# Kernel tuning notes

Measured on AMD Instinct MI355X. Metric: run time of the kernel, lower is better.

Reference implementation:

```python
import jax, jax.numpy as jnp
import numpy as np

N_NODES = 100000
N_EDGES = 4800000


def gcn_conv(x, edge_index, W, b):
    """PyG GCNConv: add self-loops, symmetric deg^-1/2 normalization, scatter-add."""
    n = x.shape[0]
    loops = jnp.arange(n, dtype=edge_index.dtype)
    src = jnp.concatenate([edge_index[0], loops])  # [E+N] message sources
    dst = jnp.concatenate([edge_index[1], loops])  # [E+N] message targets
    deg = jax.ops.segment_sum(jnp.ones_like(dst, dtype=x.dtype), dst, num_segments=n)
    dinv = jnp.where(deg > 0, jax.lax.rsqrt(deg), 0.0)  # deg^{-1/2}, guard isolated nodes
    norm = dinv[src] * dinv[dst]                  # [E+N]
    h = x @ W                                      # [N, out] tiny GEMM
    msg = h[src] * norm[:, None]                   # gather + scale (memory bound)
    out = jax.ops.segment_sum(msg, dst, num_segments=n)  # scatter-add
    return out + b


def setup_inputs() -> dict:
    key = jax.random.key(0)
    k1, k2, k3, k4 = jax.random.split(key, 4)
    node_features = jax.random.normal(k1, (N_NODES, 1), dtype=jnp.float32)
    edge_index = jax.random.randint(k2, (2, N_EDGES), 0, N_NODES, dtype=jnp.int32)
    W1 = jax.random.normal(k3, (1, 16), dtype=jnp.float32) / jnp.sqrt(1.0)
    b1 = jnp.zeros((16,), dtype=jnp.float32)
    W2 = jax.random.normal(k4, (16, 2), dtype=jnp.float32) / jnp.sqrt(16.0)
    b2 = jnp.zeros((2,), dtype=jnp.float32)
    return {"node_features": node_features, "edge_index": edge_index,
            "W1": W1, "b1": b1, "W2": W2, "b2": b2}


def reference(node_features, edge_index, W1, b1, W2, b2):
    h = gcn_conv(node_features, edge_index, W1, b1)
    h = jax.nn.relu(h)
    h = gcn_conv(h, edge_index, W2, b2)
    return jax.nn.log_softmax(h, axis=1)
```

## Files before the change

kernel.cpp:

```cpp
#include <hip/hip_runtime.h>
#include <math.h>


#define NNODES 100000
#define NEDGES 4800000
#define BN 256
#define NB 391
#define B1 512
#define CHUNK 9375
#define SRC_BITS 17
#define SRC_MASK 0x1FFFF

__global__ __launch_bounds__(512) void hist_k(const int* __restrict__ dst,
                                              int* __restrict__ blockhist, int E) {
    __shared__ int h[NB];
    int blk = blockIdx.x;
    for (int i = threadIdx.x; i < NB; i += 512) h[i] = 0;
    __syncthreads();
    int lo = blk * CHUNK, hi = lo + CHUNK; if (hi > E) hi = E;
    for (int i = lo + threadIdx.x; i < hi; i += 512) atomicAdd(&h[dst[i] >> 8], 1);
    __syncthreads();
    int* row = blockhist + (size_t)blk * NB;
    for (int i = threadIdx.x; i < NB; i += 512) row[i] = h[i];
}

__global__ __launch_bounds__(512) void scanblk_k(const int* __restrict__ blockhist,
                                                 int* __restrict__ offs,
                                                 int* __restrict__ colsum) {
    int b = blockIdx.x, t = threadIdx.x;
    int v = blockhist[(size_t)t * NB + b];
    __shared__ int ps[512];
    ps[t] = v; __syncthreads();
    for (int off = 1; off < 512; off <<= 1) {
        int add = (t >= off) ? ps[t - off] : 0;
        __syncthreads();
        ps[t] += add;
        __syncthreads();
    }
    offs[(size_t)t * NB + b] = ps[t] - v;
    if (t == 511) colsum[b] = ps[t];
}

__global__ __launch_bounds__(512) void base_k(const int* __restrict__ colsum,
                                              int* __restrict__ bucketbase) {
    __shared__ int ps[512];
    int t = threadIdx.x;
    int v = (t < NB) ? colsum[t] : 0;
    ps[t] = v; __syncthreads();
    for (int off = 1; off < 512; off <<= 1) {
        int add = (t >= off) ? ps[t - off] : 0;
        __syncthreads();
        ps[t] += add;
        __syncthreads();
    }
    if (t < NB) bucketbase[t] = ps[t] - v;
}

__global__ __launch_bounds__(512) void binfill_k(const int* __restrict__ src,
                                                 const int* __restrict__ dst,
                                                 const int* __restrict__ offs,
                                                 const int* __restrict__ bucketbase,
                                                 unsigned* __restrict__ recs, int E) {
    __shared__ int cur[NB];
    int blk = blockIdx.x;
    const int* row = offs + (size_t)blk * NB;
    for (int i = threadIdx.x; i < NB; i += 512) cur[i] = bucketbase[i] + row[i];
    __syncthreads();
    int lo = blk * CHUNK, hi = lo + CHUNK; if (hi > E) hi = E;
    for (int i = lo + threadIdx.x; i < hi; i += 512) {
        int d = dst[i];
        int b = d >> 8;
        int pos = atomicAdd(&cur[b], 1);
        recs[pos] = (unsigned)src[i] | ((unsigned)(d & (BN - 1)) << SRC_BITS);
    }
}

__global__ __launch_bounds__(512) void deg_k(const unsigned* __restrict__ recs,
                                             const int* __restrict__ bucketbase,
                                             const int* __restrict__ colsum,
                                             const float* __restrict__ x,
                                             float* __restrict__ dinv,
                                             float* __restrict__ p, int N) {
    int b = blockIdx.x;
    __shared__ int hh[BN];
    if (threadIdx.x < BN) hh[threadIdx.x] = 0;
    __syncthreads();
    int base = bucketbase[b], cnt = colsum[b];
    for (int i = threadIdx.x; i < cnt; i += 512) atomicAdd(&hh[recs[base + i] >> SRC_BITS], 1);
    __syncthreads();
    if (threadIdx.x < BN) {
        int n = b * BN + threadIdx.x;
        if (n < N) {
            float di = rsqrtf((float)(hh[threadIdx.x] + 1));
            dinv[n] = di;
            p[n] = x[n] * di;
        }
    }
}

__global__ __launch_bounds__(512) void agg1_k(const unsigned* __restrict__ recs,
                                              const int* __restrict__ bucketbase,
                                              const int* __restrict__ colsum,
                                              const float* __restrict__ dinv,
                                              const float* __restrict__ p,
                                              const float* __restrict__ W1,
                                              const float* __restrict__ b1,
                                              const float* __restrict__ W2,
                                              float2* __restrict__ g, int N) {
    int b = blockIdx.x;
    __shared__ float acc[BN];
    if (threadIdx.x < BN) acc[threadIdx.x] = 0.f;
    __syncthreads();
    int base = bucketbase[b], cnt = colsum[b];
    for (int i = threadIdx.x; i < cnt; i += 512) {
        unsigned r = recs[base + i];
        atomicAdd(&acc[r >> SRC_BITS], p[r & SRC_MASK]);
    }
    __syncthreads();
    if (threadIdx.x < BN) {
        int n = b * BN + threadIdx.x;
        if (n < N) {
            float di = dinv[n];
            float s = di * (p[n] + acc[threadIdx.x]);
            float g0 = 0.f, g1 = 0.f;
            #pragma unroll
            for (int k = 0; k < 16; ++k) {
                float h = fmaxf(fmaf(W1[k], s, b1[k]), 0.f);
                g0 = fmaf(h, W2[2 * k + 0], g0);
                g1 = fmaf(h, W2[2 * k + 1], g1);
            }
            g[n] = make_float2(g0 * di, g1 * di);
        }
    }
}

__global__ __launch_bounds__(512) void agg2_k(const unsigned* __restrict__ recs,
                                              const int* __restrict__ bucketbase,
                                              const int* __restrict__ colsum,
                                              const float* __restrict__ dinv,
                                              const float2* __restrict__ g,
                                              const float* __restrict__ b2,
                                              float2* __restrict__ out, int N) {
    int b = blockIdx.x;
    __shared__ float a0[BN], a1[BN];
    if (threadIdx.x < BN) { a0[threadIdx.x] = 0.f; a1[threadIdx.x] = 0.f; }
    __syncthreads();
    int base = bucketbase[b], cnt = colsum[b];
    for (int i = threadIdx.x; i < cnt; i += 512) {
        unsigned r = recs[base + i];
        float2 gv = g[r & SRC_MASK];
        int li = r >> SRC_BITS;
        atomicAdd(&a0[li], gv.x);
        atomicAdd(&a1[li], gv.y);
    }
    __syncthreads();
    if (threadIdx.x < BN) {
        int n = b * BN + threadIdx.x;
        if (n < N) {
            float di = dinv[n];
            float2 gv = g[n];
            float o0 = fmaf(di, gv.x + a0[threadIdx.x], b2[0]);
            float o1 = fmaf(di, gv.y + a1[threadIdx.x], b2[1]);
            float m = fmaxf(o0, o1);
            float lse = m + logf(expf(o0 - m) + expf(o1 - m));
            out[n] = make_float2(o0 - lse, o1 - lse);
        }
    }
}


__global__ void count_deg_k(const int* __restrict__ dst, int* __restrict__ degi, int E) {
    int i = blockIdx.x * blockDim.x + threadIdx.x;
    if (i < E) atomicAdd(&degi[dst[i]], 1);
}
__global__ void node1_k(const float* __restrict__ x, const int* __restrict__ degi,
                        float* __restrict__ dinv, float* __restrict__ p, int N) {
    int n = blockIdx.x * blockDim.x + threadIdx.x;
    if (n < N) {
        float di = rsqrtf((float)(degi[n] + 1));
        dinv[n] = di;
        p[n] = x[n] * di;
    }
}
__global__ void scatter1_k(const int* __restrict__ src, const int* __restrict__ dst,
                           const float* __restrict__ p, float* __restrict__ acc1, int E) {
    int i = blockIdx.x * blockDim.x + threadIdx.x;
    if (i < E) atomicAdd(&acc1[dst[i]], p[src[i]]);
}
__global__ void node2_k(const float* __restrict__ dinv, const float* __restrict__ p,
                        const float* __restrict__ acc1, const float* __restrict__ W1,
                        const float* __restrict__ b1, const float* __restrict__ W2,
                        float2* __restrict__ g, int N) {
    int n = blockIdx.x * blockDim.x + threadIdx.x;
    if (n < N) {
        float di = dinv[n];
        float s = di * (p[n] + acc1[n]);
        float g0 = 0.f, g1 = 0.f;
        #pragma unroll
        for (int k = 0; k < 16; ++k) {
            float h = fmaxf(fmaf(W1[k], s, b1[k]), 0.f);
            g0 = fmaf(h, W2[2 * k + 0], g0);
            g1 = fmaf(h, W2[2 * k + 1], g1);
        }
        g[n] = make_float2(g0 * di, g1 * di);
    }
}
__global__ void scatter2_k(const int* __restrict__ src, const int* __restrict__ dst,
                           const float2* __restrict__ g, float* __restrict__ acc2, int E) {
    int i = blockIdx.x * blockDim.x + threadIdx.x;
    if (i < E) {
        float2 gv = g[src[i]];
        int d = dst[i];
        atomicAdd(&acc2[2 * d + 0], gv.x);
        atomicAdd(&acc2[2 * d + 1], gv.y);
    }
}
__global__ void final_k(const float* __restrict__ dinv, const float2* __restrict__ g,
                        const float2* __restrict__ acc2, const float* __restrict__ b2,
                        float2* __restrict__ out, int N) {
    int n = blockIdx.x * blockDim.x + threadIdx.x;
    if (n < N) {
        float di = dinv[n];
        float2 gv = g[n];
        float2 av = acc2[n];
        float o0 = fmaf(di, gv.x + av.x, b2[0]);
        float o1 = fmaf(di, gv.y + av.y, b2[1]);
        float m = fmaxf(o0, o1);
        float lse = m + logf(expf(o0 - m) + expf(o1 - m));
        out[n] = make_float2(o0 - lse, o1 - lse);
    }
}

extern "C" void kernel_launch(void* const* d_in, const int* in_sizes, int n_in,
                              void* d_out, int out_size, void* d_ws, size_t ws_size,
                              hipStream_t stream) {
    const float* x  = (const float*)d_in[0];
    const int*   ei = (const int*)d_in[1];
    const float* W1 = (const float*)d_in[2];
    const float* b1 = (const float*)d_in[3];
    const float* W2 = (const float*)d_in[4];
    const float* b2 = (const float*)d_in[5];
    float2* out = (float2*)d_out;

    const int N = in_sizes[0];
    const int E = in_sizes[1] / 2;
    const int* src = ei;
    const int* dst = ei + E;

    size_t o_recs = 0;
    size_t o_bh   = o_recs + ((size_t)E * 4 + 255 & ~255UL);
    size_t o_offs = o_bh   + ((size_t)B1 * NB * 4 + 255 & ~255UL);
    size_t o_cs   = o_offs + ((size_t)B1 * NB * 4 + 255 & ~255UL);
    size_t o_bb   = o_cs   + ((size_t)NB * 4 + 255 & ~255UL);
    size_t o_dinv = o_bb   + ((size_t)NB * 4 + 255 & ~255UL);
    size_t o_p    = o_dinv + ((size_t)N * 4 + 255 & ~255UL);
    size_t o_g    = o_p    + ((size_t)N * 4 + 255 & ~255UL);
    size_t need   = o_g    + (size_t)N * 8;

    if (N == NNODES && E == NEDGES && ws_size >= need) {
        char* ws = (char*)d_ws;
        unsigned* recs = (unsigned*)(ws + o_recs);
        int* blockhist = (int*)(ws + o_bh);
        int* offs      = (int*)(ws + o_offs);
        int* colsum    = (int*)(ws + o_cs);
        int* bucketbase= (int*)(ws + o_bb);
        float* dinv    = (float*)(ws + o_dinv);
        float* p       = (float*)(ws + o_p);
        float2* g      = (float2*)(ws + o_g);

        hist_k   <<<B1, 512, 0, stream>>>(dst, blockhist, E);
        scanblk_k<<<NB, 512, 0, stream>>>(blockhist, offs, colsum);
        base_k   <<<1, 512, 0, stream>>>(colsum, bucketbase);
        binfill_k<<<B1, 512, 0, stream>>>(src, dst, offs, bucketbase, recs, E);
        deg_k    <<<NB, 512, 0, stream>>>(recs, bucketbase, colsum, x, dinv, p, N);
        agg1_k   <<<NB, 512, 0, stream>>>(recs, bucketbase, colsum, dinv, p, W1, b1, W2, g, N);
        agg2_k   <<<NB, 512, 0, stream>>>(recs, bucketbase, colsum, dinv, g, b2, out, N);
    } else {
        char* ws = (char*)d_ws;
        int*    degi = (int*)(ws);
        float*  acc1 = (float*)(ws + 4UL * N);
        float*  acc2 = (float*)(ws + 8UL * N);
        float*  dinv = (float*)(ws + 16UL * N);
        float*  p    = (float*)(ws + 20UL * N);
        float2* g    = (float2*)(ws + 24UL * N);
        const int B = 256;
        const int gE = (E + B - 1) / B;
        const int gN = (N + B - 1) / B;
        hipMemsetAsync(ws, 0, 16UL * N, stream);
        count_deg_k<<<gE, B, 0, stream>>>(dst, degi, E);
        node1_k<<<gN, B, 0, stream>>>(x, degi, dinv, p, N);
        scatter1_k<<<gE, B, 0, stream>>>(src, dst, p, acc1, E);
        node2_k<<<gN, B, 0, stream>>>(dinv, p, acc1, W1, b1, W2, g, N);
        scatter2_k<<<gE, B, 0, stream>>>(src, dst, g, acc2, E);
        final_k<<<gN, B, 0, stream>>>(dinv, g, (const float2*)acc2, b2, out, N);
    }
}
```

Before: 243.6 us.

## Split per-bucket aggregation across four blocks with partial-sum combine kernels

Each destination bucket's edge records are divided into four segments handled by separate blocks. Each block writes shared-memory partial sums to global buffers, and a light per-node kernel adds the four partials and runs the node-wise epilogue. This raises the grid from 391 to 1564 blocks so the many CUs of the device are better filled during the gather and shared-atomic phases. The cost is three extra kernel launches and extra global traffic for the partial buffers.

```diff
diff --git a/kernel.cpp b/kernel.cpp
--- a/kernel.cpp
+++ b/kernel.cpp
@@ -6,8 +6,10 @@
 #define NEDGES 4800000
 #define BN 256
 #define NB 391
+#define NPAD (NB * BN)
 #define B1 512
 #define CHUNK 9375
+#define SEG 4
 #define SRC_BITS 17
 #define SRC_MASK 0x1FFFF
 
@@ -75,96 +77,127 @@
     }
 }
 
-__global__ __launch_bounds__(512) void deg_k(const unsigned* __restrict__ recs,
-                                             const int* __restrict__ bucketbase,
-                                             const int* __restrict__ colsum,
-                                             const float* __restrict__ x,
-                                             float* __restrict__ dinv,
-                                             float* __restrict__ p, int N) {
-    int b = blockIdx.x;
+__global__ __launch_bounds__(512) void deg_s_k(const unsigned* __restrict__ recs,
+                                               const int* __restrict__ bucketbase,
+                                               const int* __restrict__ colsum,
+                                               int* __restrict__ dpart) {
+    int blk = blockIdx.x;
+    int b = blk >> 2, sg = blk & (SEG - 1);
     __shared__ int hh[BN];
     if (threadIdx.x < BN) hh[threadIdx.x] = 0;
     __syncthreads();
     int base = bucketbase[b], cnt = colsum[b];
-    for (int i = threadIdx.x; i < cnt; i += 512) atomicAdd(&hh[recs[base + i] >> SRC_BITS], 1);
-    __syncthreads();
-    if (threadIdx.x < BN) {
-        int n = b * BN + threadIdx.x;
-        if (n < N) {
-            float di = rsqrtf((float)(hh[threadIdx.x] + 1));
-            dinv[n] = di;
-            p[n] = x[n] * di;
-        }
-    }
-}
-
-__global__ __launch_bounds__(512) void agg1_k(const unsigned* __restrict__ recs,
-                                              const int* __restrict__ bucketbase,
-                                              const int* __restrict__ colsum,
-                                              const float* __restrict__ dinv,
-                                              const float* __restrict__ p,
-                                              const float* __restrict__ W1,
-                                              const float* __restrict__ b1,
-                                              const float* __restrict__ W2,
-                                              float2* __restrict__ g, int N) {
-    int b = blockIdx.x;
+    int lo = base + (int)((long long)cnt * sg / SEG);
+    int hi = base + (int)((long long)cnt * (sg + 1) / SEG);
+    for (int i = lo + threadIdx.x; i < hi; i += 512)
+        atomicAdd(&hh[recs[i] >> SRC_BITS], 1);
+    __syncthreads();
+    if (threadIdx.x < BN)
+        dpart[(size_t)sg * NPAD + b * BN + threadIdx.x] = hh[threadIdx.x];
+}
+
+__global__ __launch_bounds__(512) void deg_c_k(const float* __restrict__ x,
+                                               const int* __restrict__ dpart,
+                                               float* __restrict__ dinv,
+                                               float* __restrict__ p, int N) {
+    int n = blockIdx.x * blockDim.x + threadIdx.x;
+    if (n < N) {
+        int d = dpart[n] + dpart[NPAD + n] + dpart[2 * NPAD + n] + dpart[3 * NPAD + n];
+        float di = rsqrtf((float)(d + 1));
+        dinv[n] = di;
+        p[n] = x[n] * di;
+    }
+}
+
+__global__ __launch_bounds__(512) void agg1_s_k(const unsigned* __restrict__ recs,
+                                                const int* __restrict__ bucketbase,
+                                                const int* __restrict__ colsum,
+                                                const float* __restrict__ p,
+                                                float* __restrict__ a1part) {
+    int blk = blockIdx.x;
+    int b = blk >> 2, sg = blk & (SEG - 1);
     __shared__ float acc[BN];
     if (threadIdx.x < BN) acc[threadIdx.x] = 0.f;
     __syncthreads();
     int base = bucketbase[b], cnt = colsum[b];
-    for (int i = threadIdx.x; i < cnt; i += 512) {
-        unsigned r = recs[base + i];
+    int lo = base + (int)((long long)cnt * sg / SEG);
+    int hi = base + (int)((long long)cnt * (sg + 1) / SEG);
+    for (int i = lo + threadIdx.x; i < hi; i += 512) {
+        unsigned r = recs[i];
         atomicAdd(&acc[r >> SRC_BITS], p[r & SRC_MASK]);
     }
     __syncthreads();
-    if (threadIdx.x < BN) {
-        int n = b * BN + threadIdx.x;
-        if (n < N) {
-            float di = dinv[n];
-            float s = di * (p[n] + acc[threadIdx.x]);
-            float g0 = 0.f, g1 = 0.f;
-            #pragma unroll
-            for (int k = 0; k < 16; ++k) {
-                float h = fmaxf(fmaf(W1[k], s, b1[k]), 0.f);
-                g0 = fmaf(h, W2[2 * k + 0], g0);
-                g1 = fmaf(h, W2[2 * k + 1], g1);
-            }
-            g[n] = make_float2(g0 * di, g1 * di);
+    if (threadIdx.x < BN)
+        a1part[(size_t)sg * NPAD + b * BN + threadIdx.x] = acc[threadIdx.x];
+}
+
+__global__ __launch_bounds__(512) void agg1_c_k(const float* __restrict__ dinv,
+                                                const float* __restrict__ p,
+                                                const float* __restrict__ a1part,
+                                                const float* __restrict__ W1,
+                                                const float* __restrict__ b1,
+                                                const float* __restrict__ W2,
+                                                float2* __restrict__ g, int N) {
+    int n = blockIdx.x * blockDim.x + threadIdx.x;
+    if (n < N) {
+        float sum = a1part[n] + a1part[NPAD + n] + a1part[2 * NPAD + n] + a1part[3 * NPAD + n];
+        float di = dinv[n];
+        float s = di * (p[n] + sum);
+        float g0 = 0.f, g1 = 0.f;
+        #pragma unroll
+        for (int k = 0; k < 16; ++k) {
+            float h = fmaxf(fmaf(W1[k], s, b1[k]), 0.f);
+            g0 = fmaf(h, W2[2 * k + 0], g0);
+            g1 = fmaf(h, W2[2 * k + 1], g1);
         }
-    }
-}
-
-__global__ __launch_bounds__(512) void agg2_k(const unsigned* __restrict__ recs,
-                                              const int* __restrict__ bucketbase,
-                                              const int* __restrict__ colsum,
-                                              const float* __restrict__ dinv,
-                                              const float2* __restrict__ g,
-                                              const float* __restrict__ b2,
-                                              float2* __restrict__ out, int N) {
-    int b = blockIdx.x;
+        g[n] = make_float2(g0 * di, g1 * di);
+    }
+}
+
+__global__ __launch_bounds__(512) void agg2_s_k(const unsigned* __restrict__ recs,
+                                                const int* __restrict__ bucketbase,
+                                                const int* __restrict__ colsum,
+                                                const float2* __restrict__ g,
+                                                float2* __restrict__ a2part) {
+    int blk = blockIdx.x;
+    int b = blk >> 2, sg = blk & (SEG - 1);
     __shared__ float a0[BN], a1[BN];
     if (threadIdx.x < BN) { a0[threadIdx.x] = 0.f; a1[threadIdx.x] = 0.f; }
     __syncthreads();
     int base = bucketbase[b], cnt = colsum[b];
-    for (int i = threadIdx.x; i < cnt; i += 512) {
-        unsigned r = recs[base + i];
+    int lo = base + (int)((long long)cnt * sg / SEG);
+    int hi = base + (int)((long long)cnt * (sg + 1) / SEG);
+    for (int i = lo + threadIdx.x; i < hi; i += 512) {
+        unsigned r = recs[i];
         float2 gv = g[r & SRC_MASK];
         int li = r >> SRC_BITS;
         atomicAdd(&a0[li], gv.x);
         atomicAdd(&a1[li], gv.y);
     }
     __syncthreads();
-    if (threadIdx.x < BN) {
-        int n = b * BN + threadIdx.x;
-        if (n < N) {
-            float di = dinv[n];
-            float2 gv = g[n];
-            float o0 = fmaf(di, gv.x + a0[threadIdx.x], b2[0]);
-            float o1 = fmaf(di, gv.y + a1[threadIdx.x], b2[1]);
-            float m = fmaxf(o0, o1);
-            float lse = m + logf(expf(o0 - m) + expf(o1 - m));
-            out[n] = make_float2(o0 - lse, o1 - lse);
-        }
+    if (threadIdx.x < BN)
+        a2part[(size_t)sg * NPAD + b * BN + threadIdx.x] =
+            make_float2(a0[threadIdx.x], a1[threadIdx.x]);
+}
+
+__global__ __launch_bounds__(512) void agg2_c_k(const float* __restrict__ dinv,
+                                                const float2* __restrict__ g,
+                                                const float2* __restrict__ a2part,
+                                                const float* __restrict__ b2,
+                                                float2* __restrict__ out, int N) {
+    int n = blockIdx.x * blockDim.x + threadIdx.x;
+    if (n < N) {
+        float2 q0 = a2part[n], q1 = a2part[NPAD + n];
+        float2 q2 = a2part[2 * NPAD + n], q3 = a2part[3 * NPAD + n];
+        float s0 = q0.x + q1.x + q2.x + q3.x;
+        float s1 = q0.y + q1.y + q2.y + q3.y;
+        float di = dinv[n];
+        float2 gv = g[n];
+        float o0 = fmaf(di, gv.x + s0, b2[0]);
+        float o1 = fmaf(di, gv.y + s1, b2[1]);
+        float m = fmaxf(o0, o1);
+        float lse = m + logf(expf(o0 - m) + expf(o1 - m));
+        out[n] = make_float2(o0 - lse, o1 - lse);
     }
 }
 
@@ -255,7 +288,10 @@
     size_t o_dinv = o_bb   + ((size_t)NB * 4 + 255 & ~255UL);
     size_t o_p    = o_dinv + ((size_t)N * 4 + 255 & ~255UL);
     size_t o_g    = o_p    + ((size_t)N * 4 + 255 & ~255UL);
-    size_t need   = o_g    + (size_t)N * 8;
+    size_t o_dp   = o_g    + ((size_t)N * 8 + 255 & ~255UL);
+    size_t o_a1p  = o_dp   + ((size_t)SEG * NPAD * 4 + 255 & ~255UL);
+    size_t o_a2p  = o_a1p  + ((size_t)SEG * NPAD * 4 + 255 & ~255UL);
+    size_t need   = o_a2p  + (size_t)SEG * NPAD * 8;
 
     if (N == NNODES && E == NEDGES && ws_size >= need) {
         char* ws = (char*)d_ws;
@@ -267,31 +303,38 @@
         float* dinv    = (float*)(ws + o_dinv);
         float* p       = (float*)(ws + o_p);
         float2* g      = (float2*)(ws + o_g);
-
+        int* dpart     = (int*)(ws + o_dp);
+        float* a1part  = (float*)(ws + o_a1p);
+        float2* a2part = (float2*)(ws + o_a2p);
+
+        const int gN = (N + 511) / 512;
         hist_k   <<<B1, 512, 0, stream>>>(dst, blockhist, E);
         scanblk_k<<<NB, 512, 0, stream>>>(blockhist, offs, colsum);
         base_k   <<<1, 512, 0, stream>>>(colsum, bucketbase);
         binfill_k<<<B1, 512, 0, stream>>>(src, dst, offs, bucketbase, recs, E);
-        deg_k    <<<NB, 512, 0, stream>>>(recs, bucketbase, colsum, x, dinv, p, N);
-        agg1_k   <<<NB, 512, 0, stream>>>(recs, bucketbase, colsum, dinv, p, W1, b1, W2, g, N);
-        agg2_k   <<<NB, 512, 0, stream>>>(recs, bucketbase, colsum, dinv, g, b2, out, N);
+        deg_s_k  <<<NB * SEG, 512, 0, stream>>>(recs, bucketbase, colsum, dpart);
+        deg_c_k  <<<gN, 512, 0, stream>>>(x, dpart, dinv, p, N);
+        agg1_s_k <<<NB * SEG, 512, 0, stream>>>(recs, bucketbase, colsum, p, a1part);
+        agg1_c_k <<<gN, 512, 0, stream>>>(dinv, p, a1part, W1, b1, W2, g, N);
+        agg2_s_k <<<NB * SEG, 512, 0, stream>>>(recs, bucketbase, colsum, g, a2part);
+        agg2_c_k <<<gN, 512, 0, stream>>>(dinv, g, a2part, b2, out, N);
     } else {
         char* ws = (char*)d_ws;
         int*    degi = (int*)(ws);
         float*  acc1 = (float*)(ws + 4UL * N);
         float*  acc2 = (float*)(ws + 8UL * N);
-        float*  dinv = (float*)(ws + 16UL * N);
-        float*  p    = (float*)(ws + 20UL * N);
-        float2* g    = (float2*)(ws + 24UL * N);
+        float*  dinvf= (float*)(ws + 16UL * N);
+        float*  pf   = (float*)(ws + 20UL * N);
+        float2* gf   = (float2*)(ws + 24UL * N);
         const int B = 256;
         const int gE = (E + B - 1) / B;
-        const int gN = (N + B - 1) / B;
+        const int gNf = (N + B - 1) / B;
         hipMemsetAsync(ws, 0, 16UL * N, stream);
         count_deg_k<<<gE, B, 0, stream>>>(dst, degi, E);
-        node1_k<<<gN, B, 0, stream>>>(x, degi, dinv, p, N);
-        scatter1_k<<<gE, B, 0, stream>>>(src, dst, p, acc1, E);
-        node2_k<<<gN, B, 0, stream>>>(dinv, p, acc1, W1, b1, W2, g, N);
-        scatter2_k<<<gE, B, 0, stream>>>(src, dst, g, acc2, E);
-        final_k<<<gN, B, 0, stream>>>(dinv, g, (const float2*)acc2, b2, out, N);
-    }
-}
+        node1_k<<<gNf, B, 0, stream>>>(x, degi, dinvf, pf, N);
+        scatter1_k<<<gE, B, 0, stream>>>(src, dst, pf, acc1, E);
+        node2_k<<<gNf, B, 0, stream>>>(dinvf, pf, acc1, W1, b1, W2, gf, N);
+        scatter2_k<<<gE, B, 0, stream>>>(src, dst, gf, acc2, E);
+        final_k<<<gNf, B, 0, stream>>>(dinvf, gf, (const float2*)acc2, b2, out, N);
+    }
+}
```

After: 238.4 us. 2.1% less time.
